# Kernel tuning notes

Hardware: AMD Instinct MI355X
Metric: run time of the kernel (lower is better)

## Reference

```python
import jax, jax.numpy as jnp
import numpy as np

B, NT, D = 256, 301, 96
NSEG = 50


def setup_inputs() -> dict:
    key = jax.random.key(0)
    inp = jax.random.normal(key, (B, NT, D), dtype=jnp.float32)
    return {"inp": inp, "n_segments": NSEG}


def _logsig_depth2(segs):
    # segs: (B, S, L, D) -- per-segment sub-paths (piecewise linear)
    x0 = segs[:, :, :1, :]
    dx = segs[:, :, 1:, :] - segs[:, :, :-1, :]          # increments (B,S,L-1,D)
    xprev = segs[:, :, :-1, :] - x0                      # X(t-) - X(0)
    lvl1 = segs[:, :, -1, :] - segs[:, :, 0, :]          # level-1 logsig (B,S,D)
    # Level-2 signature S_ij = sum_t X_i(t-) dX_j + 0.5 sum_t dX_i dX_j;
    # log-signature level 2 is the antisymmetric part (Levy area), so the
    # symmetric 0.5 dx (x) dx term cancels and we only need M - M^T.
    M = jnp.einsum('bsti,bstj->bsij', xprev, dx)         # (B,S,D,D)
    A = 0.5 * (M - jnp.swapaxes(M, -1, -2))
    iu, ju = np.triu_indices(segs.shape[-1], k=1)
    # words/Lyndon basis at depth 2: coefficients A_ij for i<j, lexicographic
    return jnp.concatenate([lvl1, A[:, :, iu, ju]], axis=-1)


def reference(inp, n_segments):
    # n_segments is a static Python int -> segment index map built at trace time,
    # replicating: t_vec = [round(x) for x in linspace(1, nT, n_segments+1)],
    # segment i = inp[:, t_vec[i]-1 : t_vec[i+1], :]
    nT = inp.shape[1]
    t_vec = [int(round(x)) for x in np.linspace(1, nT, n_segments + 1)]
    idx = np.stack([np.arange(t_vec[i] - 1, t_vec[i + 1]) for i in range(n_segments)])  # (S, L)
    segs = inp[:, idx, :]                                # (B, S, L, D)
    return _logsig_depth2(segs)
```

## Files before the change

kernel.cpp:

```cpp
#include <hip/hip_runtime.h>

#define BB 256
#define NT_ 301
#define DD 96
#define NSEG 50
#define SEGROWS 7
#define NTRI (DD * (DD - 1) / 2)
#define OUTD (DD + NTRI)
#define CS 12


__global__ __launch_bounds__(256, 4)
void logsig_kernel(const float* __restrict__ inp, float* __restrict__ out) {
    const int bs = blockIdx.x;
    const int b  = bs / NSEG;
    const int s  = bs - b * NSEG;

    __shared__ float colp[DD * CS];

    const float* __restrict__ src = inp + ((size_t)b * NT_ + (size_t)(6 * s)) * DD;
    for (int idx = threadIdx.x; idx < SEGROWS * DD; idx += 256) {
        const int r = idx / DD;
        const int c = idx - r * DD;
        colp[c * CS + r] = src[idx];
    }
    __syncthreads();

    const int ty = threadIdx.x >> 4;
    const int tx = threadIdx.x & 15;

    float rs[6][8];
    int rowoff[6];
    #pragma unroll
    for (int ti = 0; ti < 6; ++ti) {
        const int i = 16 * ti + ty;
        const float4 lo = *reinterpret_cast<const float4*>(&colp[i * CS]);
        const float4 hi = *reinterpret_cast<const float4*>(&colp[i * CS + 4]);
        rs[ti][0] = 0.5f * lo.x; rs[ti][1] = 0.5f * lo.y;
        rs[ti][2] = 0.5f * lo.z; rs[ti][3] = 0.5f * lo.w;
        rs[ti][4] = 0.5f * hi.x; rs[ti][5] = 0.5f * hi.y;
        rs[ti][6] = 0.5f * hi.z;
        rs[ti][7] = rs[ti][6] - rs[ti][1];
        rowoff[ti] = DD + (i * (2 * DD - 1 - i)) / 2 - i - 1;
    }

    float* __restrict__ o = out + (size_t)bs * OUTD;

    #pragma unroll
    for (int tj = 0; tj < 6; ++tj) {
        const int j = 16 * tj + tx;
        const float4 lo = *reinterpret_cast<const float4*>(&colp[j * CS]);
        const float4 hi = *reinterpret_cast<const float4*>(&colp[j * CS + 4]);
        const float c0 = lo.x, c1 = lo.y, c2 = lo.z, c3 = lo.w;
        const float c4 = hi.x, c5 = hi.y, c6 = hi.z;
        const float uj = c6 - c1;
        if (ty == 0)
            o[j] = c6 - c0;
        #pragma unroll
        for (int ti = 0; ti <= tj; ++ti) {
            if (ti < tj || tx > ty) {
                float acc  = rs[ti][7] * c0 - rs[ti][0] * uj;
                acc += rs[ti][1] * c2 - rs[ti][2] * c1;
                acc += rs[ti][2] * c3 - rs[ti][3] * c2;
                acc += rs[ti][3] * c4 - rs[ti][4] * c3;
                acc += rs[ti][4] * c5 - rs[ti][5] * c4;
                acc += rs[ti][5] * c6 - rs[ti][6] * c5;
                o[rowoff[ti] + j] = acc;
            }
        }
    }
}

extern "C" void kernel_launch(void* const* d_in, const int* in_sizes, int n_in,
                              void* d_out, int out_size, void* d_ws, size_t ws_size,
                              hipStream_t stream) {
    const float* inp = (const float*)d_in[0];
    float* out = (float*)d_out;
    logsig_kernel<<<BB * NSEG, 256, 0, stream>>>(inp, out);
}
```

Baseline: 307.2 us.

## Process half a batch row per block, looping over 25 segments

```diff
diff --git a/kernel.cpp b/kernel.cpp
--- a/kernel.cpp
+++ b/kernel.cpp
@@ -4,68 +4,84 @@
 #define NT_ 301
 #define DD 96
 #define NSEG 50
-#define SEGROWS 7
 #define NTRI (DD * (DD - 1) / 2)
 #define OUTD (DD + NTRI)
-#define CS 12
+#define HSEG 25
+#define HROWS 151
+#define CSTR 154
 
 
-__global__ __launch_bounds__(256, 4)
+__global__ __launch_bounds__(512)
 void logsig_kernel(const float* __restrict__ inp, float* __restrict__ out) {
-    const int bs = blockIdx.x;
-    const int b  = bs / NSEG;
-    const int s  = bs - b * NSEG;
+    const int bh = blockIdx.x;
+    const int b  = bh >> 1;
+    const int h  = bh & 1;
 
-    __shared__ float colp[DD * CS];
+    __shared__ float colp[DD * CSTR];
 
-    const float* __restrict__ src = inp + ((size_t)b * NT_ + (size_t)(6 * s)) * DD;
-    for (int idx = threadIdx.x; idx < SEGROWS * DD; idx += 256) {
+    const float* __restrict__ src = inp + ((size_t)b * NT_ + (size_t)(150 * h)) * DD;
+    for (int idx = threadIdx.x; idx < HROWS * DD; idx += 512) {
         const int r = idx / DD;
         const int c = idx - r * DD;
-        colp[c * CS + r] = src[idx];
+        colp[c * CSTR + r] = src[idx];
     }
     __syncthreads();
 
-    const int ty = threadIdx.x >> 4;
-    const int tx = threadIdx.x & 15;
+    const int g    = threadIdx.x >> 8;
+    const int t256 = threadIdx.x & 255;
+    const int ty   = t256 >> 4;
+    const int tx   = t256 & 15;
 
-    float rs[6][8];
     int rowoff[6];
     #pragma unroll
     for (int ti = 0; ti < 6; ++ti) {
         const int i = 16 * ti + ty;
-        const float4 lo = *reinterpret_cast<const float4*>(&colp[i * CS]);
-        const float4 hi = *reinterpret_cast<const float4*>(&colp[i * CS + 4]);
-        rs[ti][0] = 0.5f * lo.x; rs[ti][1] = 0.5f * lo.y;
-        rs[ti][2] = 0.5f * lo.z; rs[ti][3] = 0.5f * lo.w;
-        rs[ti][4] = 0.5f * hi.x; rs[ti][5] = 0.5f * hi.y;
-        rs[ti][6] = 0.5f * hi.z;
-        rs[ti][7] = rs[ti][6] - rs[ti][1];
         rowoff[ti] = DD + (i * (2 * DD - 1 - i)) / 2 - i - 1;
     }
 
-    float* __restrict__ o = out + (size_t)bs * OUTD;
+    #pragma unroll 1
+    for (int sl = g; sl < HSEG; sl += 2) {
+        const int t0 = 6 * sl;
+        float* __restrict__ o = out + ((size_t)(b * NSEG + h * HSEG + sl)) * OUTD;
 
-    #pragma unroll
-    for (int tj = 0; tj < 6; ++tj) {
-        const int j = 16 * tj + tx;
-        const float4 lo = *reinterpret_cast<const float4*>(&colp[j * CS]);
-        const float4 hi = *reinterpret_cast<const float4*>(&colp[j * CS + 4]);
-        const float c0 = lo.x, c1 = lo.y, c2 = lo.z, c3 = lo.w;
-        const float c4 = hi.x, c5 = hi.y, c6 = hi.z;
-        const float uj = c6 - c1;
-        if (ty == 0)
-            o[j] = c6 - c0;
+        float rs[6][8];
         #pragma unroll
-        for (int ti = 0; ti <= tj; ++ti) {
-            if (ti < tj || tx > ty) {
-                float acc  = rs[ti][7] * c0 - rs[ti][0] * uj;
-                acc += rs[ti][1] * c2 - rs[ti][2] * c1;
-                acc += rs[ti][2] * c3 - rs[ti][3] * c2;
-                acc += rs[ti][3] * c4 - rs[ti][4] * c3;
-                acc += rs[ti][4] * c5 - rs[ti][5] * c4;
-                acc += rs[ti][5] * c6 - rs[ti][6] * c5;
-                o[rowoff[ti] + j] = acc;
+        for (int ti = 0; ti < 6; ++ti) {
+            const int i = 16 * ti + ty;
+            const float2* __restrict__ p =
+                reinterpret_cast<const float2*>(&colp[i * CSTR + t0]);
+            const float2 v0 = p[0], v1 = p[1], v2 = p[2];
+            const float  v6 = colp[i * CSTR + t0 + 6];
+            rs[ti][0] = 0.5f * v0.x; rs[ti][1] = 0.5f * v0.y;
+            rs[ti][2] = 0.5f * v1.x; rs[ti][3] = 0.5f * v1.y;
+            rs[ti][4] = 0.5f * v2.x; rs[ti][5] = 0.5f * v2.y;
+            rs[ti][6] = 0.5f * v6;
+            rs[ti][7] = rs[ti][6] - rs[ti][1];
+        }
+
+        #pragma unroll
+        for (int tj = 0; tj < 6; ++tj) {
+            const int j = 16 * tj + tx;
+            const float2* __restrict__ q =
+                reinterpret_cast<const float2*>(&colp[j * CSTR + t0]);
+            const float2 w0 = q[0], w1 = q[1], w2 = q[2];
+            const float  c0 = w0.x, c1 = w0.y, c2 = w1.x, c3 = w1.y;
+            const float  c4 = w2.x, c5 = w2.y;
+            const float  c6 = colp[j * CSTR + t0 + 6];
+            const float  uj = c6 - c1;
+            if (ty == 0)
+                o[j] = c6 - c0;
+            #pragma unroll
+            for (int ti = 0; ti <= tj; ++ti) {
+                if (ti < tj || tx > ty) {
+                    float acc  = rs[ti][7] * c0 - rs[ti][0] * uj;
+                    acc += rs[ti][1] * c2 - rs[ti][2] * c1;
+                    acc += rs[ti][2] * c3 - rs[ti][3] * c2;
+                    acc += rs[ti][3] * c4 - rs[ti][4] * c3;
+                    acc += rs[ti][4] * c5 - rs[ti][5] * c4;
+                    acc += rs[ti][5] * c6 - rs[ti][6] * c5;
+                    o[rowoff[ti] + j] = acc;
+                }
             }
         }
     }
@@ -76,5 +92,5 @@
                               hipStream_t stream) {
     const float* inp = (const float*)d_in[0];
     float* out = (float*)d_out;
-    logsig_kernel<<<BB * NSEG, 256, 0, stream>>>(inp, out);
+    logsig_kernel<<<2 * BB, 512, 0, stream>>>(inp, out);
 }
```

Result: faster. 300.3 us, median of 2 (-2.2%).

## Process five segments per block with float4 loads into shared memory

Applied to the files above, without the earlier changes.

```diff
diff --git a/kernel.cpp b/kernel.cpp
--- a/kernel.cpp
+++ b/kernel.cpp
@@ -4,68 +4,90 @@
 #define NT_ 301
 #define DD 96
 #define NSEG 50
-#define SEGROWS 7
 #define NTRI (DD * (DD - 1) / 2)
 #define OUTD (DD + NTRI)
+#define CHUNK 5
+#define NCH (NSEG / CHUNK)
+#define CROWS (6 * CHUNK + 1)
 #define CS 12
+#define SEGF (DD * CS)
 
 
-__global__ __launch_bounds__(256, 4)
+__global__ __launch_bounds__(256, 5)
 void logsig_kernel(const float* __restrict__ inp, float* __restrict__ out) {
-    const int bs = blockIdx.x;
-    const int b  = bs / NSEG;
-    const int s  = bs - b * NSEG;
+    const int bc = blockIdx.x;
+    const int b  = bc / NCH;
+    const int ch = bc - b * NCH;
 
-    __shared__ float colp[DD * CS];
+    __shared__ float segp[CHUNK * SEGF];
 
-    const float* __restrict__ src = inp + ((size_t)b * NT_ + (size_t)(6 * s)) * DD;
-    for (int idx = threadIdx.x; idx < SEGROWS * DD; idx += 256) {
-        const int r = idx / DD;
-        const int c = idx - r * DD;
-        colp[c * CS + r] = src[idx];
+    const float4* __restrict__ src4 = reinterpret_cast<const float4*>(
+        inp + ((size_t)b * NT_ + (size_t)(30 * ch)) * DD);
+    for (int idx = threadIdx.x; idx < CROWS * (DD / 4); idx += 256) {
+        const int r  = idx / (DD / 4);
+        const int q4 = idx - r * (DD / 4);
+        const float4 v = src4[idx];
+        const int sl_hi = min(r / 6, CHUNK - 1);
+        const int sl_lo = (r - 1) / 6;
+        for (int sl = sl_lo; sl <= sl_hi; ++sl) {
+            const int t = r - 6 * sl;
+            float* d = &segp[sl * SEGF + (q4 * 4) * CS + t];
+            d[0] = v.x; d[CS] = v.y; d[2 * CS] = v.z; d[3 * CS] = v.w;
+        }
     }
     __syncthreads();
 
     const int ty = threadIdx.x >> 4;
     const int tx = threadIdx.x & 15;
 
-    float rs[6][8];
     int rowoff[6];
     #pragma unroll
     for (int ti = 0; ti < 6; ++ti) {
         const int i = 16 * ti + ty;
-        const float4 lo = *reinterpret_cast<const float4*>(&colp[i * CS]);
-        const float4 hi = *reinterpret_cast<const float4*>(&colp[i * CS + 4]);
-        rs[ti][0] = 0.5f * lo.x; rs[ti][1] = 0.5f * lo.y;
-        rs[ti][2] = 0.5f * lo.z; rs[ti][3] = 0.5f * lo.w;
-        rs[ti][4] = 0.5f * hi.x; rs[ti][5] = 0.5f * hi.y;
-        rs[ti][6] = 0.5f * hi.z;
-        rs[ti][7] = rs[ti][6] - rs[ti][1];
         rowoff[ti] = DD + (i * (2 * DD - 1 - i)) / 2 - i - 1;
     }
 
-    float* __restrict__ o = out + (size_t)bs * OUTD;
+    float* __restrict__ obase = out + ((size_t)b * NSEG + (size_t)ch * CHUNK) * OUTD;
 
-    #pragma unroll
-    for (int tj = 0; tj < 6; ++tj) {
-        const int j = 16 * tj + tx;
-        const float4 lo = *reinterpret_cast<const float4*>(&colp[j * CS]);
-        const float4 hi = *reinterpret_cast<const float4*>(&colp[j * CS + 4]);
-        const float c0 = lo.x, c1 = lo.y, c2 = lo.z, c3 = lo.w;
-        const float c4 = hi.x, c5 = hi.y, c6 = hi.z;
-        const float uj = c6 - c1;
-        if (ty == 0)
-            o[j] = c6 - c0;
+    #pragma unroll 1
+    for (int sl = 0; sl < CHUNK; ++sl) {
+        const float* __restrict__ sp = &segp[sl * SEGF];
+        float* __restrict__ o = obase + (size_t)sl * OUTD;
+
+        float rs[6][8];
         #pragma unroll
-        for (int ti = 0; ti <= tj; ++ti) {
-            if (ti < tj || tx > ty) {
-                float acc  = rs[ti][7] * c0 - rs[ti][0] * uj;
-                acc += rs[ti][1] * c2 - rs[ti][2] * c1;
-                acc += rs[ti][2] * c3 - rs[ti][3] * c2;
-                acc += rs[ti][3] * c4 - rs[ti][4] * c3;
-                acc += rs[ti][4] * c5 - rs[ti][5] * c4;
-                acc += rs[ti][5] * c6 - rs[ti][6] * c5;
-                o[rowoff[ti] + j] = acc;
+        for (int ti = 0; ti < 6; ++ti) {
+            const int i = 16 * ti + ty;
+            const float4 lo = *reinterpret_cast<const float4*>(&sp[i * CS]);
+            const float4 hi = *reinterpret_cast<const float4*>(&sp[i * CS + 4]);
+            rs[ti][0] = 0.5f * lo.x; rs[ti][1] = 0.5f * lo.y;
+            rs[ti][2] = 0.5f * lo.z; rs[ti][3] = 0.5f * lo.w;
+            rs[ti][4] = 0.5f * hi.x; rs[ti][5] = 0.5f * hi.y;
+            rs[ti][6] = 0.5f * hi.z;
+            rs[ti][7] = rs[ti][6] - rs[ti][1];
+        }
+
+        #pragma unroll
+        for (int tj = 0; tj < 6; ++tj) {
+            const int j = 16 * tj + tx;
+            const float4 lo = *reinterpret_cast<const float4*>(&sp[j * CS]);
+            const float4 hi = *reinterpret_cast<const float4*>(&sp[j * CS + 4]);
+            const float c0 = lo.x, c1 = lo.y, c2 = lo.z, c3 = lo.w;
+            const float c4 = hi.x, c5 = hi.y, c6 = hi.z;
+            const float uj = c6 - c1;
+            if (ty == 0)
+                o[j] = c6 - c0;
+            #pragma unroll
+            for (int ti = 0; ti <= tj; ++ti) {
+                if (ti < tj || tx > ty) {
+                    float acc  = rs[ti][7] * c0 - rs[ti][0] * uj;
+                    acc += rs[ti][1] * c2 - rs[ti][2] * c1;
+                    acc += rs[ti][2] * c3 - rs[ti][3] * c2;
+                    acc += rs[ti][3] * c4 - rs[ti][4] * c3;
+                    acc += rs[ti][4] * c5 - rs[ti][5] * c4;
+                    acc += rs[ti][5] * c6 - rs[ti][6] * c5;
+                    o[rowoff[ti] + j] = acc;
+                }
             }
         }
     }
@@ -76,5 +98,5 @@
                               hipStream_t stream) {
     const float* inp = (const float*)d_in[0];
     float* out = (float*)d_out;
-    logsig_kernel<<<BB * NSEG, 256, 0, stream>>>(inp, out);
+    logsig_kernel<<<BB * NCH, 256, 0, stream>>>(inp, out);
 }
```

New measurement: 348.0 us. 13.3% more time.
